# Optimization experiments

Measured on AMD Instinct MI355X. Metric: run time of the kernel, lower is better.

## Reference

```python
import jax, jax.numpy as jnp
import numpy as np

D = 256
N_CELL = 100000
N_NET = 50000
E = 300000
EPS = 1e-5


def _agg_mean(src_feat, edge_index, num_dst):
    # edge_index[0]=src, edge_index[1]=dst; gather + segment-sum + degree-normalize
    src_idx, dst_idx = edge_index[0], edge_index[1]
    summed = jax.ops.segment_sum(src_feat[src_idx], dst_idx, num_segments=num_dst)
    deg = jax.ops.segment_sum(jnp.ones((src_idx.shape[0], 1), src_feat.dtype), dst_idx, num_segments=num_dst)
    return summed / jnp.maximum(deg, 1.0)


def _mlp(x, w1, b1, w2, b2):
    return jax.nn.relu(x @ w1 + b1) @ w2 + b2


def _layernorm(x, g, b):
    mu = jnp.mean(x, axis=-1, keepdims=True)
    var = jnp.var(x, axis=-1, keepdims=True)
    return (x - mu) * jax.lax.rsqrt(var + EPS) * g + b


def setup_inputs() -> dict:
    key = jax.random.key(0)
    ks = jax.random.split(key, 24)
    inp = {
        'cell_h': jax.random.normal(ks[0], (N_CELL, D), jnp.float32),
        'net_h': jax.random.normal(ks[1], (N_NET, D), jnp.float32),
        'cell_to_net_edge_index': jax.random.randint(ks[2], (2, E), 0, 50000),
        'net_to_cell_edge_index': jax.random.randint(ks[3], (2, E), 0, 50000),
        'cell_to_cell_edge_index': jax.random.randint(ks[4], (2, E), 0, 50000),
    }
    def lin(k, fin, fout):
        return jax.random.normal(k, (fin, fout), jnp.float32) * 0.02
    for i, name in enumerate(['c2n', 'n2c', 'c2c']):
        inp[name + '_w1'] = lin(ks[5 + 4 * i], 2 * D, D)
        inp[name + '_b1'] = jnp.zeros((D,), jnp.float32)
        inp[name + '_w2'] = lin(ks[6 + 4 * i], D, D)
        inp[name + '_b2'] = jnp.zeros((D,), jnp.float32)
    inp['net_ln_g'] = jnp.ones((D,), jnp.float32)
    inp['net_ln_b'] = jnp.zeros((D,), jnp.float32)
    inp['cell_ln_g'] = jnp.ones((D,), jnp.float32)
    inp['cell_ln_b'] = jnp.zeros((D,), jnp.float32)
    return inp


def reference(cell_h, net_h, cell_to_net_edge_index, net_to_cell_edge_index,
              cell_to_cell_edge_index,
              c2n_w1, c2n_b1, c2n_w2, c2n_b2,
              n2c_w1, n2c_b1, n2c_w2, n2c_b2,
              c2c_w1, c2c_b1, c2c_w2, c2c_b2,
              net_ln_g, net_ln_b, cell_ln_g, cell_ln_b):
    # cells -> nets
    msg_c2n = _agg_mean(cell_h, cell_to_net_edge_index, net_h.shape[0])
    net_h = _layernorm(net_h + _mlp(jnp.concatenate([net_h, msg_c2n], axis=-1),
                                    c2n_w1, c2n_b1, c2n_w2, c2n_b2),
                       net_ln_g, net_ln_b)
    # nets -> cells
    msg_n2c = _agg_mean(net_h, net_to_cell_edge_index, cell_h.shape[0])
    cell_h = cell_h + _mlp(jnp.concatenate([cell_h, msg_n2c], axis=-1),
                           n2c_w1, n2c_b1, n2c_w2, n2c_b2)
    # cells -> cells
    msg_c2c = _agg_mean(cell_h, cell_to_cell_edge_index, cell_h.shape[0])
    cell_h = cell_h + _mlp(jnp.concatenate([cell_h, msg_c2c], axis=-1),
                           c2c_w1, c2c_b1, c2c_w2, c2c_b2)
    cell_h = _layernorm(cell_h, cell_ln_g, cell_ln_b)
    return (cell_h, net_h)
```

## Files before the change

### kernel.cpp

```cpp
#include <hip/hip_runtime.h>
#include <stdint.h>

typedef unsigned short u16;
typedef short short8 __attribute__((ext_vector_type(8)));
typedef float floatx4 __attribute__((ext_vector_type(4)));

#define D_FEAT 256

__device__ __forceinline__ u16 f2bf(float x){
  unsigned u = __float_as_uint(x);
  u += 0x7FFFu + ((u >> 16) & 1u);
  return (u16)(u >> 16);
}

__device__ __forceinline__ short8 pack8(float4 a, float4 b){
  short8 v;
  v[0]=(short)f2bf(a.x); v[1]=(short)f2bf(a.y); v[2]=(short)f2bf(a.z); v[3]=(short)f2bf(a.w);
  v[4]=(short)f2bf(b.x); v[5]=(short)f2bf(b.y); v[6]=(short)f2bf(b.z); v[7]=(short)f2bf(b.w);
  return v;
}

__global__ void conv_t_kernel(const float* __restrict__ w, u16* __restrict__ wt, int K, int N){
  int idx = blockIdx.x * 256 + threadIdx.x;
  if (idx >= K * N) return;
  int k = idx / N, n = idx - k * N;
  wt[(size_t)n * K + k] = f2bf(w[idx]);
}

__global__ void hist_kernel(const int* __restrict__ didx, int E, int* __restrict__ cnt){
  int e = blockIdx.x * 256 + threadIdx.x;
  if (e < E) atomicAdd(&cnt[didx[e]], 1);
}

__global__ void scan_block_kernel(const int* __restrict__ cnt, int* __restrict__ excl,
                                  int* __restrict__ bsums, int N){
  __shared__ int tmp[256];
  int t = threadIdx.x;
  int i = blockIdx.x * 256 + t;
  int v = (i < N) ? cnt[i] : 0;
  tmp[t] = v; __syncthreads();
#pragma unroll
  for (int o = 1; o < 256; o <<= 1){
    int x = (t >= o) ? tmp[t - o] : 0;
    __syncthreads();
    tmp[t] += x;
    __syncthreads();
  }
  if (i < N) excl[i] = tmp[t] - v;
  if (t == 255) bsums[blockIdx.x] = tmp[255];
}

__global__ void scan_bsums_kernel(int* __restrict__ bsums, int nb){
  __shared__ int tmp[512];
  int t = threadIdx.x;
  if (nb > 512){
    if (t == 0){
      int acc = 0;
      for (int i = 0; i < nb; i++){ int v = bsums[i]; bsums[i] = acc; acc += v; }
    }
    return;
  }
  int v = (t < nb) ? bsums[t] : 0;
  tmp[t] = v; __syncthreads();
#pragma unroll
  for (int o = 1; o < 512; o <<= 1){
    int x = (t >= o) ? tmp[t - o] : 0;
    __syncthreads();
    tmp[t] += x;
    __syncthreads();
  }
  if (t < nb) bsums[t] = tmp[t] - v;
}

__global__ void scan_add_kernel(int* __restrict__ excl, const int* __restrict__ bsums, int N){
  int i = blockIdx.x * 256 + threadIdx.x;
  if (i < N) excl[i] += bsums[blockIdx.x];
}

__global__ void fill_csr_kernel(const int* __restrict__ sidx, const int* __restrict__ didx, int E,
                                const int* __restrict__ row_start, int* __restrict__ fillc,
                                int* __restrict__ esrc){
  int e = blockIdx.x * 256 + threadIdx.x;
  if (e >= E) return;
  int d = didx[e];
  int pos = atomicAdd(&fillc[d], 1);
  esrc[row_start[d] + pos] = sidx[e];
}

__global__ void agg_mean_kernel(const float* __restrict__ feat, const int* __restrict__ row_start,
                                const int* __restrict__ cnt, const int* __restrict__ esrc,
                                float* __restrict__ mean, int M){
  int row = blockIdx.x * 4 + (threadIdx.x >> 6);
  int lane = threadIdx.x & 63;
  if (row >= M) return;
  int beg = row_start[row], n = cnt[row];
  float4 a0 = {0.f,0.f,0.f,0.f}, a1 = {0.f,0.f,0.f,0.f};
  int j = 0;
  for (; j + 1 < n; j += 2){
    int s0 = esrc[beg + j], s1 = esrc[beg + j + 1];
    float4 v0 = ((const float4*)(feat + (size_t)s0 * D_FEAT))[lane];
    float4 v1 = ((const float4*)(feat + (size_t)s1 * D_FEAT))[lane];
    a0.x += v0.x; a0.y += v0.y; a0.z += v0.z; a0.w += v0.w;
    a1.x += v1.x; a1.y += v1.y; a1.z += v1.z; a1.w += v1.w;
  }
  if (j < n){
    int s0 = esrc[beg + j];
    float4 v0 = ((const float4*)(feat + (size_t)s0 * D_FEAT))[lane];
    a0.x += v0.x; a0.y += v0.y; a0.z += v0.z; a0.w += v0.w;
  }
  float inv = 1.0f / fmaxf((float)n, 1.0f);
  float4 o;
  o.x = (a0.x + a1.x) * inv; o.y = (a0.y + a1.y) * inv;
  o.z = (a0.z + a1.z) * inv; o.w = (a0.w + a1.w) * inv;
  ((float4*)(mean + (size_t)row * D_FEAT))[lane] = o;
}

template<int HAS_LN>
__global__ __launch_bounds__(256, 2) void fused_mlp_kernel(
    const float* __restrict__ h, const float* __restrict__ s,
    const u16* __restrict__ B1t, const float* __restrict__ b1,
    const u16* __restrict__ B2t, const float* __restrict__ b2,
    const float* __restrict__ resid,
    const float* __restrict__ lng, const float* __restrict__ lnb,
    float* __restrict__ out, int M)
{
  __shared__ short8 As8[64 * 5];
  __shared__ short8 Bs8[256 * 5];
  __shared__ u16 hid[64][264];
  __shared__ float part[2][64][4];

  int tid = threadIdx.x;
  int wave = tid >> 6, lane = tid & 63;
  int half = lane >> 4, l16 = lane & 15;
  int wc = wave * 64;
  int row0 = blockIdx.x * 64;

  int rA = tid >> 2, uA = tid & 3;
  int rgA = row0 + rA;

  floatx4 acc[4][4];
  floatx4 zero4 = {0.f, 0.f, 0.f, 0.f};
#pragma unroll
  for (int i = 0; i < 4; i++)
#pragma unroll
    for (int j = 0; j < 4; j++) acc[i][j] = zero4;

  float4 pa0 = {0.f,0.f,0.f,0.f}, pa1 = {0.f,0.f,0.f,0.f};
  short8 pb[4];

  {
    int kk = uA * 8;
    if (rgA < M){
      const float* src = h + (size_t)rgA * 256 + kk;
      pa0 = ((const float4*)src)[0];
      pa1 = ((const float4*)src)[1];
    }
#pragma unroll
    for (int cc = 0; cc < 4; cc++){
      int c = tid + cc * 256;
      int r = c >> 2, u = c & 3;
      pb[cc] = *(const short8*)(B1t + (size_t)r * 512 + u * 8);
    }
  }

  for (int k0 = 0; k0 < 512; k0 += 32){
    {
      short8 va = {0,0,0,0,0,0,0,0};
      if (rgA < M) va = pack8(pa0, pa1);
      As8[rA * 5 + uA] = va;
    }
#pragma unroll
    for (int cc = 0; cc < 4; cc++){
      int c = tid + cc * 256;
      int r = c >> 2, u = c & 3;
      Bs8[r * 5 + u] = pb[cc];
    }
    __syncthreads();

    if (k0 < 480){
      int k0n = k0 + 32;
      int kk = k0n + uA * 8;
      if (rgA < M){
        const float* src = (kk < 256) ? (h + (size_t)rgA * 256 + kk)
                                      : (s + (size_t)rgA * 256 + (kk - 256));
        pa0 = ((const float4*)src)[0];
        pa1 = ((const float4*)src)[1];
      }
#pragma unroll
      for (int cc = 0; cc < 4; cc++){
        int c = tid + cc * 256;
        int r = c >> 2, u = c & 3;
        pb[cc] = *(const short8*)(B1t + (size_t)r * 512 + k0n + u * 8);
      }
    }

    short8 af[4], bfr[4];
#pragma unroll
    for (int t = 0; t < 4; t++){
      af[t]  = As8[(t * 16 + l16) * 5 + half];
      bfr[t] = Bs8[(wc + t * 16 + l16) * 5 + half];
    }
#pragma unroll
    for (int i = 0; i < 4; i++)
#pragma unroll
      for (int j = 0; j < 4; j++)
        acc[i][j] = __builtin_amdgcn_mfma_f32_16x16x32_bf16(af[i], bfr[j], acc[i][j], 0, 0, 0);
    __syncthreads();
  }

#pragma unroll
  for (int i = 0; i < 4; i++){
#pragma unroll
    for (int j = 0; j < 4; j++){
      int cg = wc + j * 16 + l16;
      float bv = b1[cg];
#pragma unroll
      for (int r = 0; r < 4; r++){
        int lr = i * 16 + half * 4 + r;
        hid[lr][cg] = f2bf(fmaxf(acc[i][j][r] + bv, 0.0f));
      }
    }
  }

#pragma unroll
  for (int i = 0; i < 4; i++)
#pragma unroll
    for (int j = 0; j < 4; j++) acc[i][j] = zero4;

#pragma unroll
  for (int cc = 0; cc < 4; cc++){
    int c = tid + cc * 256;
    int r = c >> 2, u = c & 3;
    pb[cc] = *(const short8*)(B2t + (size_t)r * 256 + u * 8);
  }

  for (int k0 = 0; k0 < 256; k0 += 32){
#pragma unroll
    for (int cc = 0; cc < 4; cc++){
      int c = tid + cc * 256;
      int r = c >> 2, u = c & 3;
      Bs8[r * 5 + u] = pb[cc];
    }
    __syncthreads();

    if (k0 < 224){
      int k0n = k0 + 32;
#pragma unroll
      for (int cc = 0; cc < 4; cc++){
        int c = tid + cc * 256;
        int r = c >> 2, u = c & 3;
        pb[cc] = *(const short8*)(B2t + (size_t)r * 256 + k0n + u * 8);
      }
    }

    short8 af[4], bfr[4];
#pragma unroll
    for (int t = 0; t < 4; t++){
      af[t]  = *(const short8*)(&hid[t * 16 + l16][k0 + half * 8]);
      bfr[t] = Bs8[(wc + t * 16 + l16) * 5 + half];
    }
#pragma unroll
    for (int i = 0; i < 4; i++)
#pragma unroll
      for (int j = 0; j < 4; j++)
        acc[i][j] = __builtin_amdgcn_mfma_f32_16x16x32_bf16(af[i], bfr[j], acc[i][j], 0, 0, 0);
    __syncthreads();
  }

#pragma unroll
  for (int i = 0; i < 4; i++){
#pragma unroll
    for (int j = 0; j < 4; j++){
      int cg = wc + j * 16 + l16;
      float bv = b2[cg];
#pragma unroll
      for (int r = 0; r < 4; r++){
        int lr = i * 16 + half * 4 + r;
        int rg = row0 + lr;
        float rv = (rg < M) ? resid[(size_t)rg * 256 + cg] : 0.0f;
        acc[i][j][r] = acc[i][j][r] + bv + rv;
      }
    }
  }

  if (HAS_LN){
#pragma unroll
    for (int i = 0; i < 4; i++){
#pragma unroll
      for (int r = 0; r < 4; r++){
        float s1 = 0.f, s2 = 0.f;
#pragma unroll
        for (int j = 0; j < 4; j++){
          float v = acc[i][j][r];
          s1 += v; s2 += v * v;
        }
#pragma unroll
        for (int m = 1; m < 16; m <<= 1){
          s1 += __shfl_xor(s1, m, 64);
          s2 += __shfl_xor(s2, m, 64);
        }
        if (l16 == 0){
          int lr = i * 16 + half * 4 + r;
          part[0][lr][wave] = s1;
          part[1][lr][wave] = s2;
        }
      }
    }
    __syncthreads();
#pragma unroll
    for (int i = 0; i < 4; i++){
#pragma unroll
      for (int r = 0; r < 4; r++){
        int lr = i * 16 + half * 4 + r;
        int rg = row0 + lr;
        float4 p1 = *(const float4*)part[0][lr];
        float4 p2 = *(const float4*)part[1][lr];
        float su = p1.x + p1.y + p1.z + p1.w;
        float sq = p2.x + p2.y + p2.z + p2.w;
        float mean = su * (1.0f / 256.0f);
        float var = sq * (1.0f / 256.0f) - mean * mean;
        float rs = rsqrtf(var + 1e-5f);
        if (rg < M){
#pragma unroll
          for (int j = 0; j < 4; j++){
            int cg = wc + j * 16 + l16;
            float vv = (acc[i][j][r] - mean) * rs * lng[cg] + lnb[cg];
            out[(size_t)rg * 256 + cg] = vv;
          }
        }
      }
    }
  } else {
#pragma unroll
    for (int i = 0; i < 4; i++){
#pragma unroll
      for (int r = 0; r < 4; r++){
        int lr = i * 16 + half * 4 + r;
        int rg = row0 + lr;
        if (rg < M){
#pragma unroll
          for (int j = 0; j < 4; j++){
            int cg = wc + j * 16 + l16;
            out[(size_t)rg * 256 + cg] = acc[i][j][r];
          }
        }
      }
    }
  }
}

static void run_agg(const float* feat, const int* edge, int E, int Ndst,
                    int* cnt, int* row_start, int* fillc, int* bsums, int* esrc,
                    float* mean, hipStream_t stream){
  const int* sidx = edge;
  const int* didx = edge + E;
  hipMemsetAsync(cnt, 0, (size_t)Ndst * 4, stream);
  hipMemsetAsync(fillc, 0, (size_t)Ndst * 4, stream);
  int egrid = (E + 255) / 256;
  hist_kernel<<<egrid, 256, 0, stream>>>(didx, E, cnt);
  int nb = (Ndst + 255) / 256;
  scan_block_kernel<<<nb, 256, 0, stream>>>(cnt, row_start, bsums, Ndst);
  scan_bsums_kernel<<<1, 512, 0, stream>>>(bsums, nb);
  scan_add_kernel<<<nb, 256, 0, stream>>>(row_start, bsums, Ndst);
  fill_csr_kernel<<<egrid, 256, 0, stream>>>(sidx, didx, E, row_start, fillc, esrc);
  agg_mean_kernel<<<(Ndst + 3) / 4, 256, 0, stream>>>(feat, row_start, cnt, esrc, mean, Ndst);
}

extern "C" void kernel_launch(void* const* d_in, const int* in_sizes, int n_in,
                              void* d_out, int out_size, void* d_ws, size_t ws_size,
                              hipStream_t stream){
  const float* cell_h = (const float*)d_in[0];
  const float* net_h  = (const float*)d_in[1];
  const int* e_c2n = (const int*)d_in[2];
  const int* e_n2c = (const int*)d_in[3];
  const int* e_c2c = (const int*)d_in[4];
  const float* w1p[3] = {(const float*)d_in[5], (const float*)d_in[9],  (const float*)d_in[13]};
  const float* b1p[3] = {(const float*)d_in[6], (const float*)d_in[10], (const float*)d_in[14]};
  const float* w2p[3] = {(const float*)d_in[7], (const float*)d_in[11], (const float*)d_in[15]};
  const float* b2p[3] = {(const float*)d_in[8], (const float*)d_in[12], (const float*)d_in[16]};
  const float* net_g  = (const float*)d_in[17];
  const float* net_b  = (const float*)d_in[18];
  const float* cell_g = (const float*)d_in[19];
  const float* cell_b = (const float*)d_in[20];

  int n_cell = in_sizes[0] / 256;
  int n_net  = in_sizes[1] / 256;
  int E = in_sizes[2] / 2;

  float* cell_out = (float*)d_out;
  float* net_out  = (float*)d_out + (size_t)n_cell * 256;

  char* p = (char*)d_ws;
  u16* w1t[3]; u16* w2t[3];
  for (int i = 0; i < 3; i++){
    w1t[i] = (u16*)p; p += (size_t)512 * 256 * 2;
    w2t[i] = (u16*)p; p += (size_t)256 * 256 * 2;
  }
  float* Mbuf = (float*)p; p += (size_t)n_cell * 256 * 4;
  int n_pad = ((n_cell + 63) / 64) * 64;
  int* cnt       = (int*)p; p += (size_t)n_pad * 4;
  int* row_start = (int*)p; p += (size_t)n_pad * 4;
  int* fillc     = (int*)p; p += (size_t)n_pad * 4;
  int* bsums     = (int*)p; p += 1024 * 4;
  int* esrc      = (int*)p; p += (size_t)E * 4;

  for (int i = 0; i < 3; i++){
    conv_t_kernel<<<(512 * 256 + 255) / 256, 256, 0, stream>>>(w1p[i], w1t[i], 512, 256);
    conv_t_kernel<<<(256 * 256 + 255) / 256, 256, 0, stream>>>(w2p[i], w2t[i], 256, 256);
  }

  dim3 blk(256);

  run_agg(cell_h, e_c2n, E, n_net, cnt, row_start, fillc, bsums, esrc, Mbuf, stream);
  fused_mlp_kernel<1><<<dim3((n_net + 63) / 64), blk, 0, stream>>>(
      net_h, Mbuf, w1t[0], b1p[0], w2t[0], b2p[0], net_h, net_g, net_b, net_out, n_net);

  run_agg(net_out, e_n2c, E, n_cell, cnt, row_start, fillc, bsums, esrc, Mbuf, stream);
  fused_mlp_kernel<0><<<dim3((n_cell + 63) / 64), blk, 0, stream>>>(
      cell_h, Mbuf, w1t[1], b1p[1], w2t[1], b2p[1], cell_h, nullptr, nullptr, cell_out, n_cell);

  run_agg(cell_out, e_c2c, E, n_cell, cnt, row_start, fillc, bsums, esrc, Mbuf, stream);
  fused_mlp_kernel<1><<<dim3((n_cell + 63) / 64), blk, 0, stream>>>(
      cell_out, Mbuf, w1t[2], b1p[2], w2t[2], b2p[2], cell_out, cell_g, cell_b, cell_out, n_cell);
}
```

Measured before the change: 841.6 us.

## Store aggregated means as bf16 and XOR-swizzle MLP shared memory

The mean-aggregation kernel now writes bf16 instead of fp32, halving the memory traffic of the message buffer that the fused MLP reads. The MLP kernel's shared-memory tiles switch from padded layouts to XOR-swizzled layouts packed into one aliased buffer. The launch bound is raised to three blocks per CU for more occupancy. This risks register pressure or spills under the tighter register cap, and rounds the mean before the divide-free pack.

```diff
diff --git a/kernel.cpp b/kernel.cpp
--- a/kernel.cpp
+++ b/kernel.cpp
@@ -3,6 +3,7 @@
 
 typedef unsigned short u16;
 typedef short short8 __attribute__((ext_vector_type(8)));
+typedef short short4v __attribute__((ext_vector_type(4)));
 typedef float floatx4 __attribute__((ext_vector_type(4)));
 
 #define D_FEAT 256
@@ -89,7 +90,7 @@
 
 __global__ void agg_mean_kernel(const float* __restrict__ feat, const int* __restrict__ row_start,
                                 const int* __restrict__ cnt, const int* __restrict__ esrc,
-                                float* __restrict__ mean, int M){
+                                u16* __restrict__ mean, int M){
   int row = blockIdx.x * 4 + (threadIdx.x >> 6);
   int lane = threadIdx.x & 63;
   if (row >= M) return;
@@ -109,25 +110,28 @@
     a0.x += v0.x; a0.y += v0.y; a0.z += v0.z; a0.w += v0.w;
   }
   float inv = 1.0f / fmaxf((float)n, 1.0f);
-  float4 o;
-  o.x = (a0.x + a1.x) * inv; o.y = (a0.y + a1.y) * inv;
-  o.z = (a0.z + a1.z) * inv; o.w = (a0.w + a1.w) * inv;
-  ((float4*)(mean + (size_t)row * D_FEAT))[lane] = o;
+  short4v o;
+  o[0] = (short)f2bf((a0.x + a1.x) * inv);
+  o[1] = (short)f2bf((a0.y + a1.y) * inv);
+  o[2] = (short)f2bf((a0.z + a1.z) * inv);
+  o[3] = (short)f2bf((a0.w + a1.w) * inv);
+  ((short4v*)(mean + (size_t)row * D_FEAT))[lane] = o;
 }
 
 template<int HAS_LN>
-__global__ __launch_bounds__(256, 2) void fused_mlp_kernel(
-    const float* __restrict__ h, const float* __restrict__ s,
+__global__ __launch_bounds__(256, 3) void fused_mlp_kernel(
+    const float* __restrict__ h, const u16* __restrict__ s,
     const u16* __restrict__ B1t, const float* __restrict__ b1,
     const u16* __restrict__ B2t, const float* __restrict__ b2,
     const float* __restrict__ resid,
     const float* __restrict__ lng, const float* __restrict__ lnb,
     float* __restrict__ out, int M)
 {
-  __shared__ short8 As8[64 * 5];
-  __shared__ short8 Bs8[256 * 5];
-  __shared__ u16 hid[64][264];
-  __shared__ float part[2][64][4];
+  __shared__ __align__(16) char smem_raw[53248];
+  short8* As8 = (short8*)smem_raw;
+  short8* Bs8 = (short8*)(smem_raw + 4096);
+  u16*    hid = (u16*)(smem_raw + 20480);
+  float*  part = (float*)smem_raw;
 
   int tid = threadIdx.x;
   int wave = tid >> 6, lane = tid & 63;
@@ -137,6 +141,7 @@
 
   int rA = tid >> 2, uA = tid & 3;
   int rgA = row0 + rA;
+  int aw_idx = (rA << 2) | (uA ^ (rA & 3));
 
   floatx4 acc[4][4];
   floatx4 zero4 = {0.f, 0.f, 0.f, 0.f};
@@ -146,7 +151,8 @@
     for (int j = 0; j < 4; j++) acc[i][j] = zero4;
 
   float4 pa0 = {0.f,0.f,0.f,0.f}, pa1 = {0.f,0.f,0.f,0.f};
-  short8 pb[4];
+  short8 ps = {0,0,0,0,0,0,0,0};
+  short8 pbv[4];
 
   {
     int kk = uA * 8;
@@ -159,46 +165,53 @@
     for (int cc = 0; cc < 4; cc++){
       int c = tid + cc * 256;
       int r = c >> 2, u = c & 3;
-      pb[cc] = *(const short8*)(B1t + (size_t)r * 512 + u * 8);
+      pbv[cc] = *(const short8*)(B1t + (size_t)r * 512 + u * 8);
     }
   }
 
   for (int k0 = 0; k0 < 512; k0 += 32){
     {
       short8 va = {0,0,0,0,0,0,0,0};
-      if (rgA < M) va = pack8(pa0, pa1);
-      As8[rA * 5 + uA] = va;
+      if (k0 < 256){ if (rgA < M) va = pack8(pa0, pa1); }
+      else         { va = ps; }
+      As8[aw_idx] = va;
     }
 #pragma unroll
     for (int cc = 0; cc < 4; cc++){
       int c = tid + cc * 256;
       int r = c >> 2, u = c & 3;
-      Bs8[r * 5 + u] = pb[cc];
+      Bs8[(r << 2) | (u ^ (r & 3))] = pbv[cc];
     }
     __syncthreads();
 
     if (k0 < 480){
       int k0n = k0 + 32;
       int kk = k0n + uA * 8;
-      if (rgA < M){
-        const float* src = (kk < 256) ? (h + (size_t)rgA * 256 + kk)
-                                      : (s + (size_t)rgA * 256 + (kk - 256));
-        pa0 = ((const float4*)src)[0];
-        pa1 = ((const float4*)src)[1];
+      if (k0n < 256){
+        if (rgA < M){
+          const float* src = h + (size_t)rgA * 256 + kk;
+          pa0 = ((const float4*)src)[0];
+          pa1 = ((const float4*)src)[1];
+        }
+      } else {
+        ps = (rgA < M) ? *(const short8*)(s + (size_t)rgA * 256 + (kk - 256))
+                       : (short8){0,0,0,0,0,0,0,0};
       }
 #pragma unroll
       for (int cc = 0; cc < 4; cc++){
         int c = tid + cc * 256;
         int r = c >> 2, u = c & 3;
-        pb[cc] = *(const short8*)(B1t + (size_t)r * 512 + k0n + u * 8);
+        pbv[cc] = *(const short8*)(B1t + (size_t)r * 512 + k0n + u * 8);
       }
     }
 
     short8 af[4], bfr[4];
 #pragma unroll
     for (int t = 0; t < 4; t++){
-      af[t]  = As8[(t * 16 + l16) * 5 + half];
-      bfr[t] = Bs8[(wc + t * 16 + l16) * 5 + half];
+      int ra = t * 16 + l16;
+      af[t] = As8[(ra << 2) | (half ^ (ra & 3))];
+      int rb = wc + t * 16 + l16;
+      bfr[t] = Bs8[(rb << 2) | (half ^ (rb & 3))];
     }
 #pragma unroll
     for (int i = 0; i < 4; i++)
@@ -217,7 +230,8 @@
 #pragma unroll
       for (int r = 0; r < 4; r++){
         int lr = i * 16 + half * 4 + r;
-        hid[lr][cg] = f2bf(fmaxf(acc[i][j][r] + bv, 0.0f));
+        int idx = lr * 256 + ((((cg >> 3) ^ (lr & 7)) << 3) | (cg & 7));
+        hid[idx] = f2bf(fmaxf(acc[i][j][r] + bv, 0.0f));
       }
     }
   }
@@ -231,7 +245,7 @@
   for (int cc = 0; cc < 4; cc++){
     int c = tid + cc * 256;
     int r = c >> 2, u = c & 3;
-    pb[cc] = *(const short8*)(B2t + (size_t)r * 256 + u * 8);
+    pbv[cc] = *(const short8*)(B2t + (size_t)r * 256 + u * 8);
   }
 
   for (int k0 = 0; k0 < 256; k0 += 32){
@@ -239,7 +253,7 @@
     for (int cc = 0; cc < 4; cc++){
       int c = tid + cc * 256;
       int r = c >> 2, u = c & 3;
-      Bs8[r * 5 + u] = pb[cc];
+      Bs8[(r << 2) | (u ^ (r & 3))] = pbv[cc];
     }
     __syncthreads();
 
@@ -249,15 +263,18 @@
       for (int cc = 0; cc < 4; cc++){
         int c = tid + cc * 256;
         int r = c >> 2, u = c & 3;
-        pb[cc] = *(const short8*)(B2t + (size_t)r * 256 + k0n + u * 8);
+        pbv[cc] = *(const short8*)(B2t + (size_t)r * 256 + k0n + u * 8);
       }
     }
 
     short8 af[4], bfr[4];
 #pragma unroll
     for (int t = 0; t < 4; t++){
-      af[t]  = *(const short8*)(&hid[t * 16 + l16][k0 + half * 8]);
-      bfr[t] = Bs8[(wc + t * 16 + l16) * 5 + half];
+      int ra = t * 16 + l16;
+      int chunkL = (k0 >> 3) + half;
+      af[t] = *(const short8*)(hid + ra * 256 + ((chunkL ^ (ra & 7)) << 3));
+      int rb = wc + t * 16 + l16;
+      bfr[t] = Bs8[(rb << 2) | (half ^ (rb & 3))];
     }
 #pragma unroll
     for (int i = 0; i < 4; i++)
@@ -301,8 +318,8 @@
         }
         if (l16 == 0){
           int lr = i * 16 + half * 4 + r;
-          part[0][lr][wave] = s1;
-          part[1][lr][wave] = s2;
+          part[lr * 4 + wave]       = s1;
+          part[256 + lr * 4 + wave] = s2;
         }
       }
     }
@@ -313,8 +330,8 @@
       for (int r = 0; r < 4; r++){
         int lr = i * 16 + half * 4 + r;
         int rg = row0 + lr;
-        float4 p1 = *(const float4*)part[0][lr];
-        float4 p2 = *(const float4*)part[1][lr];
+        float4 p1 = *(const float4*)(part + lr * 4);
+        float4 p2 = *(const float4*)(part + 256 + lr * 4);
         float su = p1.x + p1.y + p1.z + p1.w;
         float sq = p2.x + p2.y + p2.z + p2.w;
         float mean = su * (1.0f / 256.0f);
@@ -351,7 +368,7 @@
 
 static void run_agg(const float* feat, const int* edge, int E, int Ndst,
                     int* cnt, int* row_start, int* fillc, int* bsums, int* esrc,
-                    float* mean, hipStream_t stream){
+                    u16* mean, hipStream_t stream){
   const int* sidx = edge;
   const int* didx = edge + E;
   hipMemsetAsync(cnt, 0, (size_t)Ndst * 4, stream);
@@ -396,7 +413,7 @@
     w1t[i] = (u16*)p; p += (size_t)512 * 256 * 2;
     w2t[i] = (u16*)p; p += (size_t)256 * 256 * 2;
   }
-  float* Mbuf = (float*)p; p += (size_t)n_cell * 256 * 4;
+  u16* Mbuf = (u16*)p; p += (size_t)n_cell * 256 * 2;
   int n_pad = ((n_cell + 63) / 64) * 64;
   int* cnt       = (int*)p; p += (size_t)n_pad * 4;
   int* row_start = (int*)p; p += (size_t)n_pad * 4;
```

New measurement: 812.5 us. -3.5%, faster.
